# Optimization experiments

Hardware: AMD Instinct MI355X
Metric: run time of the kernel (lower is better)

## Reference

```python
import jax, jax.numpy as jnp
import numpy as np

B, M, N, E, H, HID = 4, 512, 512, 256, 16, 16
D = E // H


def setup_inputs() -> dict:
    key = jax.random.key(0)
    ks = jax.random.split(key, 10)
    u = lambda k, shape, lim: jax.random.uniform(k, shape, jnp.float32, -lim, lim)
    mix1_init = (1.0 / 2.0) ** 0.5
    mix2_init = (1.0 / 16.0) ** 0.5
    return {
        "q_input": jax.random.normal(ks[0], (B, M, E), jnp.float32),
        "kv_input": jax.random.normal(ks[1], (B, N, E), jnp.float32),
        "dmat": jax.random.uniform(ks[2], (B, M, N), jnp.float32),
        "Wq": u(ks[3], (E, E), 1.0 / np.sqrt(E)),
        "Wkv": u(ks[4], (2 * E, E), 1.0 / np.sqrt(E)),
        "mix_W1": u(ks[5], (H, 2, HID), mix1_init),
        "mix_b1": u(ks[6], (H, HID), mix1_init),
        "mix_W2": u(ks[7], (H, HID, 1), mix2_init),
        "mix_b2": u(ks[8], (H, 1), mix2_init),
        "Wout": u(ks[9], (E, E), 1.0 / np.sqrt(E)),
    }


def reference(q_input, kv_input, dmat, Wq, Wkv, mix_W1, mix_b1, mix_W2, mix_b2, Wout):
    b, m, e = q_input.shape
    n = kv_input.shape[1]
    h = mix_W1.shape[0]
    d = e // h
    # projections (torch Linear: y = x @ W.T)
    q = (q_input @ Wq.T).reshape(b, m, h, d).transpose(0, 2, 1, 3)        # b h m d
    kv = (kv_input @ Wkv.T).reshape(b, n, 2, h, d)                        # (two h d) split
    k = kv[:, :, 0].transpose(0, 2, 1, 3)                                 # b h n d
    v = kv[:, :, 1].transpose(0, 2, 1, 3)                                 # b h n d
    scale = jnp.sqrt(jnp.asarray(d, q.dtype))
    scores = jnp.einsum('bhmd,bhnd->bhmn', q, k) / scale                  # b h m n
    # mix scores with dmat via per-head 2-layer MLP on the last (size-2) axis
    mix = jnp.stack([scores, jnp.broadcast_to(dmat[:, None], scores.shape)], axis=-1)  # b h m n 2
    hidden = jax.nn.relu(jnp.einsum('bhmnt,htk->bhmnk', mix, mix_W1)
                         + mix_b1[None, :, None, None, :])                # b h m n HID
    mixed = (jnp.einsum('bhmnk,hko->bhmno', hidden, mix_W2)
             + mix_b2[None, :, None, None, :])[..., 0]                    # b h m n
    probs = jax.nn.softmax(mixed, axis=-1)
    out = jnp.einsum('bhmn,bhnd->bhmd', probs, v)                         # b h m d
    out = out.transpose(0, 2, 1, 3).reshape(b, m, e)                      # b m (h d)
    return out @ Wout.T
```

## Files before the change

### kernel.cpp

```cpp
#include <hip/hip_runtime.h>
#include <stdint.h>
#include <stddef.h>

#define MM 512
#define NN 512
#define EE 256
#define HH 16
#define DD 16

typedef __bf16 bf16x8 __attribute__((ext_vector_type(8)));
typedef float f32x4 __attribute__((ext_vector_type(4)));

static __device__ __forceinline__ bf16x8 bzero8() {
  bf16x8 z;
#pragma unroll
  for (int i = 0; i < 8; ++i) z[i] = (__bf16)0.0f;
  return z;
}

static __device__ __forceinline__ bf16x8 cvt8(const float* __restrict__ p) {
  const float4 u = *(const float4*)p;
  const float4 v = *(const float4*)(p + 4);
  bf16x8 r;
  r[0] = (__bf16)u.x; r[1] = (__bf16)u.y; r[2] = (__bf16)u.z; r[3] = (__bf16)u.w;
  r[4] = (__bf16)v.x; r[5] = (__bf16)v.y; r[6] = (__bf16)v.z; r[7] = (__bf16)v.w;
  return r;
}

static __device__ __forceinline__ unsigned short f2b(float f) {
  union { __bf16 h; unsigned short u; } cv;
  cv.h = (__bf16)f;
  return cv.u;
}

static __device__ __forceinline__ float b2f(unsigned short u) {
  union { unsigned int i; float f; } cv;
  cv.i = ((unsigned int)u) << 16;
  return cv.f;
}

static __device__ __forceinline__ float fexp2(float x) {
  float r;
  asm("v_exp_f32 %0, %1" : "=v"(r) : "v"(x));
  return r;
}

static __device__ __forceinline__ float sload(const float* p) {
  return __int_as_float(__builtin_amdgcn_readfirstlane(__float_as_int(*p)));
}

__global__ __launch_bounds__(256) void proj_all_kernel(
    const float* __restrict__ Xq, const float* __restrict__ Xkv,
    const float* __restrict__ Wq, const float* __restrict__ Wkv,
    const float* __restrict__ Wout,
    unsigned short* __restrict__ Qs, unsigned short* __restrict__ Ks,
    unsigned short* __restrict__ Vt,
    unsigned short* __restrict__ Whi, unsigned short* __restrict__ Wlo) {
  const int by = blockIdx.y;
  const int tid = threadIdx.x;

  if (by == 12) {
    const int base = (blockIdx.x * 256 + tid) * 4;
    const float4 v = *(const float4*)(Wout + base);
    float c[4] = {v.x, v.y, v.z, v.w};
#pragma unroll
    for (int i = 0; i < 4; ++i) {
      const unsigned short hb = f2b(c[i]);
      Whi[base + i] = hb;
      Wlo[base + i] = f2b(c[i] - b2f(hb));
    }
    return;
  }

  const int w = tid >> 6, l = tid & 63;
  const int lg = l >> 4, lr = l & 15;
  const int t0 = blockIdx.x * 32 + (w & 1) * 16;

  if (by < 4) {
    const int n0 = by * 64 + (w >> 1) * 32;
    f32x4 acc0 = {0.f, 0.f, 0.f, 0.f}, acc1 = {0.f, 0.f, 0.f, 0.f};
#pragma unroll
    for (int kc = 0; kc < EE; kc += 32) {
      const int k = kc + lg * 8;
      bf16x8 a  = cvt8(Xq + (size_t)(t0 + lr) * EE + k);
      bf16x8 b0 = cvt8(Wq + (size_t)(n0 + lr) * EE + k);
      bf16x8 b1 = cvt8(Wq + (size_t)(n0 + 16 + lr) * EE + k);
      acc0 = __builtin_amdgcn_mfma_f32_16x16x32_bf16(a, b0, acc0, 0, 0, 0);
      acc1 = __builtin_amdgcn_mfma_f32_16x16x32_bf16(a, b1, acc1, 0, 0, 0);
    }
#pragma unroll
    for (int r = 0; r < 4; ++r) {
      const int t = t0 + 4 * lg + r, b = t >> 9, m = t & 511;
      const int j0 = n0 + lr, j1 = j0 + 16;
      Qs[((size_t)(b * HH + (j0 >> 4)) * MM + m) * DD + (j0 & 15)] = f2b(acc0[r] * 0.25f);
      Qs[((size_t)(b * HH + (j1 >> 4)) * MM + m) * DD + (j1 & 15)] = f2b(acc1[r] * 0.25f);
    }
  } else {
    const int n0 = (by - 4) * 64 + (w >> 1) * 32;
    f32x4 acc0 = {0.f, 0.f, 0.f, 0.f}, acc1 = {0.f, 0.f, 0.f, 0.f};
#pragma unroll
    for (int kc = 0; kc < EE; kc += 32) {
      const int k = kc + lg * 8;
      bf16x8 a  = cvt8(Xkv + (size_t)(t0 + lr) * EE + k);
      bf16x8 b0 = cvt8(Wkv + (size_t)(n0 + lr) * EE + k);
      bf16x8 b1 = cvt8(Wkv + (size_t)(n0 + 16 + lr) * EE + k);
      acc0 = __builtin_amdgcn_mfma_f32_16x16x32_bf16(a, b0, acc0, 0, 0, 0);
      acc1 = __builtin_amdgcn_mfma_f32_16x16x32_bf16(a, b1, acc1, 0, 0, 0);
    }
#pragma unroll
    for (int r = 0; r < 4; ++r) {
      const int t = t0 + 4 * lg + r, b = t >> 9, n = t & 511;
#pragma unroll
      for (int fi = 0; fi < 2; ++fi) {
        const int j = n0 + lr + fi * 16;
        const float v = fi ? acc1[r] : acc0[r];
        if (j < 256) {
          Ks[((size_t)(b * HH + (j >> 4)) * NN + n) * DD + (j & 15)] = f2b(v);
        } else {
          const int jj = j - 256;
          Vt[((size_t)(b * HH + (jj >> 4)) * DD + (jj & 15)) * NN + n] = f2b(v);
        }
      }
    }
  }
}

__global__ __launch_bounds__(256) void attn_kernel(
    const unsigned short* __restrict__ Qs, const unsigned short* __restrict__ Ks,
    const unsigned short* __restrict__ Vt, const float* __restrict__ dmat,
    const float* __restrict__ W1, const float* __restrict__ b1v,
    const float* __restrict__ W2,
    unsigned short* __restrict__ Ahi, unsigned short* __restrict__ Alo) {
  __shared__ unsigned short P[32][520];
  __shared__ float red[4][32];
  __shared__ float pvred[4][2][16][16];

  const int tid = threadIdx.x, w = tid >> 6, l = tid & 63;
  const int lg = l >> 4, lr = l & 15;
  const int bid = blockIdx.x;
  const int mt = bid & 15, hh = (bid >> 4) & 15, b = bid >> 8;
  const int m0 = mt * 32;
  const int n0 = w * 128;

  const unsigned short* Qbase = Qs + ((size_t)(b * HH + hh) * MM + m0) * DD;
  const unsigned short* Kbase = Ks + (size_t)(b * HH + hh) * NN * DD;
  const unsigned short* Vbase = Vt + (size_t)(b * HH + hh) * DD * NN;
  const float* dbase = dmat + (size_t)b * MM * NN;

  bf16x8 qa[2];
#pragma unroll
  for (int mb = 0; mb < 2; ++mb) {
    qa[mb] = bzero8();
    if (lg < 2) qa[mb] = *(const bf16x8*)(Qbase + (mb * 16 + lr) * DD + lg * 8);
  }

  f32x4 zf = {0.f, 0.f, 0.f, 0.f};
  f32x4 c[2][8];
#pragma unroll
  for (int mb = 0; mb < 2; ++mb)
#pragma unroll
    for (int nb = 0; nb < 8; ++nb) c[mb][nb] = zf;

#pragma unroll
  for (int nb = 0; nb < 8; ++nb) {
    bf16x8 kb = bzero8();
    if (lg < 2)
      kb = *(const bf16x8*)(Kbase + (size_t)(n0 + nb * 16 + lr) * DD + lg * 8);
    c[0][nb] = __builtin_amdgcn_mfma_f32_16x16x32_bf16(qa[0], kb, c[0][nb], 0, 0, 0);
    c[1][nb] = __builtin_amdgcn_mfma_f32_16x16x32_bf16(qa[1], kb, c[1][nb], 0, 0, 0);
  }

  float ak[16], ck[16], bk[16], wk[16];
  float Ac = 0.f, Cc = 0.f;
  const float hiln2 = 0.5f * 1.4426950408889634f;
#pragma unroll
  for (int k = 0; k < 16; ++k) {
    ak[k] = sload(W1 + hh * 32 + k);
    ck[k] = sload(W1 + hh * 32 + 16 + k);
    bk[k] = sload(b1v + hh * 16 + k);
    wk[k] = hiln2 * sload(W2 + hh * 16 + k);
    Ac += wk[k] * ak[k];
    Cc += wk[k] * ck[k];
  }

  float psum[2][4] = {};
#pragma unroll
  for (int mb = 0; mb < 2; ++mb) {
    const int mrow = m0 + mb * 16 + 4 * lg;
#pragma unroll
    for (int nb = 0; nb < 8; ++nb) {
      const int ncol = n0 + nb * 16 + lr;
      const float* dp = dbase + (size_t)mrow * NN + ncol;
      float dv[4];
#pragma unroll
      for (int r = 0; r < 4; ++r) dv[r] = dp[(size_t)r * NN];
#pragma unroll
      for (int r = 0; r < 4; ++r) {
        const float s = c[mb][nb][r];
        const float d = dv[r];
        float acc = fmaf(Ac, s, Cc * d);
#pragma unroll
        for (int k = 0; k < 16; ++k) {
          const float t = fmaf(ak[k], s, fmaf(ck[k], d, bk[k]));
          acc = fmaf(wk[k], fabsf(t), acc);
        }
        const float e = fexp2(acc);
        psum[mb][r] += e;
        P[mb * 16 + 4 * lg + r][n0 + nb * 16 + lr] = f2b(e);
      }
    }
  }

#pragma unroll
  for (int mb = 0; mb < 2; ++mb)
#pragma unroll
    for (int r = 0; r < 4; ++r) {
#pragma unroll
      for (int off = 8; off > 0; off >>= 1)
        psum[mb][r] += __shfl_xor(psum[mb][r], off, 16);
      if (lr == 0) red[w][mb * 16 + 4 * lg + r] = psum[mb][r];
    }

  f32x4 pv[2];
  pv[0] = zf; pv[1] = zf;
#pragma unroll
  for (int kb = 0; kb < 4; ++kb) {
    const bf16x8 vb = *(const bf16x8*)(Vbase + (size_t)lr * NN + (n0 + kb * 32 + lg * 8));
#pragma unroll
    for (int mb = 0; mb < 2; ++mb) {
      const bf16x8 pa = *(const bf16x8*)(&P[mb * 16 + lr][n0 + kb * 32 + lg * 8]);
      pv[mb] = __builtin_amdgcn_mfma_f32_16x16x32_bf16(pa, vb, pv[mb], 0, 0, 0);
    }
  }
#pragma unroll
  for (int mb = 0; mb < 2; ++mb)
#pragma unroll
    for (int r = 0; r < 4; ++r) pvred[w][mb][4 * lg + r][lr] = pv[mb][r];
  __syncthreads();

  for (int i = tid; i < 512; i += 256) {
    const int mr = i >> 4, dd = i & 15;
    const float s = pvred[0][mr >> 4][mr & 15][dd] + pvred[1][mr >> 4][mr & 15][dd] +
                    pvred[2][mr >> 4][mr & 15][dd] + pvred[3][mr >> 4][mr & 15][dd];
    const float rs = red[0][mr] + red[1][mr] + red[2][mr] + red[3][mr];
    const float val = s / rs;
    const unsigned short hb = f2b(val);
    const size_t o = ((size_t)(b * MM) + m0 + mr) * EE + hh * DD + dd;
    Ahi[o] = hb;
    Alo[o] = f2b(val - b2f(hb));
  }
}

__global__ __launch_bounds__(256) void out_gemm_kernel(
    const unsigned short* __restrict__ Ahi, const unsigned short* __restrict__ Alo,
    const unsigned short* __restrict__ Whi, const unsigned short* __restrict__ Wlo,
    float* __restrict__ out) {
  const int tid = threadIdx.x, w = tid >> 6, l = tid & 63;
  const int lg = l >> 4, lr = l & 15;
  const int t0 = blockIdx.x * 32 + (w & 1) * 16;
  const int n0 = blockIdx.y * 64 + (w >> 1) * 32;
  f32x4 acc0 = {0.f, 0.f, 0.f, 0.f}, acc1 = {0.f, 0.f, 0.f, 0.f};
#pragma unroll
  for (int kc = 0; kc < EE; kc += 32) {
    const int k = kc + lg * 8;
    const bf16x8 ah = *(const bf16x8*)(Ahi + (size_t)(t0 + lr) * EE + k);
    const bf16x8 al = *(const bf16x8*)(Alo + (size_t)(t0 + lr) * EE + k);
    const bf16x8 bh0 = *(const bf16x8*)(Whi + (size_t)(n0 + lr) * EE + k);
    const bf16x8 bh1 = *(const bf16x8*)(Whi + (size_t)(n0 + 16 + lr) * EE + k);
    const bf16x8 bl0 = *(const bf16x8*)(Wlo + (size_t)(n0 + lr) * EE + k);
    const bf16x8 bl1 = *(const bf16x8*)(Wlo + (size_t)(n0 + 16 + lr) * EE + k);
    acc0 = __builtin_amdgcn_mfma_f32_16x16x32_bf16(ah, bh0, acc0, 0, 0, 0);
    acc0 = __builtin_amdgcn_mfma_f32_16x16x32_bf16(al, bh0, acc0, 0, 0, 0);
    acc0 = __builtin_amdgcn_mfma_f32_16x16x32_bf16(ah, bl0, acc0, 0, 0, 0);
    acc1 = __builtin_amdgcn_mfma_f32_16x16x32_bf16(ah, bh1, acc1, 0, 0, 0);
    acc1 = __builtin_amdgcn_mfma_f32_16x16x32_bf16(al, bh1, acc1, 0, 0, 0);
    acc1 = __builtin_amdgcn_mfma_f32_16x16x32_bf16(ah, bl1, acc1, 0, 0, 0);
  }
#pragma unroll
  for (int r = 0; r < 4; ++r) {
    const int row = t0 + 4 * lg + r;
    out[(size_t)row * EE + n0 + lr] = acc0[r];
    out[(size_t)row * EE + n0 + 16 + lr] = acc1[r];
  }
}

extern "C" void kernel_launch(void* const* d_in, const int* in_sizes, int n_in,
                              void* d_out, int out_size, void* d_ws, size_t ws_size,
                              hipStream_t stream) {
  const float* q_input  = (const float*)d_in[0];
  const float* kv_input = (const float*)d_in[1];
  const float* dmat     = (const float*)d_in[2];
  const float* Wq       = (const float*)d_in[3];
  const float* Wkv      = (const float*)d_in[4];
  const float* W1       = (const float*)d_in[5];
  const float* b1       = (const float*)d_in[6];
  const float* W2       = (const float*)d_in[7];
  const float* Wout     = (const float*)d_in[9];
  float* out = (float*)d_out;

  char* ws = (char*)d_ws;
  unsigned short* Qs  = (unsigned short*)(ws);
  unsigned short* Ks  = (unsigned short*)(ws + (1u << 20));
  unsigned short* Vt  = (unsigned short*)(ws + (2u << 20));
  unsigned short* Ahi = (unsigned short*)(ws + (3u << 20));
  unsigned short* Alo = (unsigned short*)(ws + (4u << 20));
  unsigned short* Whi = (unsigned short*)(ws + (5u << 20));
  unsigned short* Wlo = (unsigned short*)(ws + (5u << 20) + (1u << 17));

  proj_all_kernel<<<dim3(64, 13), 256, 0, stream>>>(q_input, kv_input, Wq, Wkv, Wout,
                                                    Qs, Ks, Vt, Whi, Wlo);
  attn_kernel<<<dim3(1024), 256, 0, stream>>>(Qs, Ks, Vt, dmat, W1, b1, W2, Ahi, Alo);
  out_gemm_kernel<<<dim3(64, 4), 256, 0, stream>>>(Ahi, Alo, Whi, Wlo, out);
}
```

Measured before the change: 63.78 us.

## Refactor mix MLP algebra, transpose score MFMA, fuse per-block S/P loop

```diff
diff --git a/kernel.cpp b/kernel.cpp
--- a/kernel.cpp
+++ b/kernel.cpp
@@ -42,6 +42,12 @@
 static __device__ __forceinline__ float fexp2(float x) {
   float r;
   asm("v_exp_f32 %0, %1" : "=v"(r) : "v"(x));
+  return r;
+}
+
+static __device__ __forceinline__ unsigned int cvtpk(float lo, float hi) {
+  unsigned int r;
+  asm("v_cvt_pk_bf16_f32 %0, %1, %2" : "=v"(r) : "v"(lo), "v"(hi));
   return r;
 }
 
@@ -62,12 +68,12 @@
   if (by == 12) {
     const int base = (blockIdx.x * 256 + tid) * 4;
     const float4 v = *(const float4*)(Wout + base);
-    float c[4] = {v.x, v.y, v.z, v.w};
+    float c4[4] = {v.x, v.y, v.z, v.w};
 #pragma unroll
     for (int i = 0; i < 4; ++i) {
-      const unsigned short hb = f2b(c[i]);
+      const unsigned short hb = f2b(c4[i]);
       Whi[base + i] = hb;
-      Wlo[base + i] = f2b(c[i] - b2f(hb));
+      Wlo[base + i] = f2b(c4[i] - b2f(hb));
     }
     return;
   }
@@ -125,7 +131,7 @@
   }
 }
 
-__global__ __launch_bounds__(256) void attn_kernel(
+__global__ __launch_bounds__(256, 4) void attn_kernel(
     const unsigned short* __restrict__ Qs, const unsigned short* __restrict__ Ks,
     const unsigned short* __restrict__ Vt, const float* __restrict__ dmat,
     const float* __restrict__ W1, const float* __restrict__ b1v,
@@ -133,7 +139,7 @@
     unsigned short* __restrict__ Ahi, unsigned short* __restrict__ Alo) {
   __shared__ unsigned short P[32][520];
   __shared__ float red[4][32];
-  __shared__ float pvred[4][2][16][16];
+  float (*pvred)[2][16][16] = (float (*)[2][16][16]) & P[0][0];
 
   const int tid = threadIdx.x, w = tid >> 6, l = tid & 63;
   const int lg = l >> 4, lr = l & 15;
@@ -147,79 +153,72 @@
   const unsigned short* Vbase = Vt + (size_t)(b * HH + hh) * DD * NN;
   const float* dbase = dmat + (size_t)b * MM * NN;
 
-  bf16x8 qa[2];
-#pragma unroll
-  for (int mb = 0; mb < 2; ++mb) {
-    qa[mb] = bzero8();
-    if (lg < 2) qa[mb] = *(const bf16x8*)(Qbase + (mb * 16 + lr) * DD + lg * 8);
-  }
-
-  f32x4 zf = {0.f, 0.f, 0.f, 0.f};
-  f32x4 c[2][8];
-#pragma unroll
-  for (int mb = 0; mb < 2; ++mb)
-#pragma unroll
-    for (int nb = 0; nb < 8; ++nb) c[mb][nb] = zf;
-
-#pragma unroll
-  for (int nb = 0; nb < 8; ++nb) {
-    bf16x8 kb = bzero8();
-    if (lg < 2)
-      kb = *(const bf16x8*)(Kbase + (size_t)(n0 + nb * 16 + lr) * DD + lg * 8);
-    c[0][nb] = __builtin_amdgcn_mfma_f32_16x16x32_bf16(qa[0], kb, c[0][nb], 0, 0, 0);
-    c[1][nb] = __builtin_amdgcn_mfma_f32_16x16x32_bf16(qa[1], kb, c[1][nb], 0, 0, 0);
-  }
-
-  float ak[16], ck[16], bk[16], wk[16];
+  float ckp[16], bkp[16], wkp[16];
   float Ac = 0.f, Cc = 0.f;
   const float hiln2 = 0.5f * 1.4426950408889634f;
 #pragma unroll
   for (int k = 0; k < 16; ++k) {
-    ak[k] = sload(W1 + hh * 32 + k);
-    ck[k] = sload(W1 + hh * 32 + 16 + k);
-    bk[k] = sload(b1v + hh * 16 + k);
-    wk[k] = hiln2 * sload(W2 + hh * 16 + k);
-    Ac += wk[k] * ak[k];
-    Cc += wk[k] * ck[k];
-  }
-
-  float psum[2][4] = {};
+    const float ak = sload(W1 + hh * 32 + k);
+    const float ck = sload(W1 + hh * 32 + 16 + k);
+    const float bk = sload(b1v + hh * 16 + k);
+    const float wk = hiln2 * sload(W2 + hh * 16 + k);
+    Ac += wk * ak;
+    Cc += wk * ck;
+    const float ra = 1.0f / ak;
+    ckp[k] = ck * ra;
+    bkp[k] = bk * ra;
+    wkp[k] = wk * fabsf(ak);
+  }
+
+  bf16x8 qb[2];
 #pragma unroll
   for (int mb = 0; mb < 2; ++mb) {
-    const int mrow = m0 + mb * 16 + 4 * lg;
-#pragma unroll
-    for (int nb = 0; nb < 8; ++nb) {
-      const int ncol = n0 + nb * 16 + lr;
-      const float* dp = dbase + (size_t)mrow * NN + ncol;
-      float dv[4];
-#pragma unroll
-      for (int r = 0; r < 4; ++r) dv[r] = dp[(size_t)r * NN];
+    qb[mb] = bzero8();
+    if (lg < 2) qb[mb] = *(const bf16x8*)(Qbase + (mb * 16 + lr) * DD + lg * 8);
+  }
+
+  const f32x4 zf = {0.f, 0.f, 0.f, 0.f};
+  float psum[2] = {0.f, 0.f};
+
+#pragma unroll
+  for (int nb = 0; nb < 8; ++nb) {
+    bf16x8 ka = bzero8();
+    if (lg < 2)
+      ka = *(const bf16x8*)(Kbase + (size_t)(n0 + nb * 16 + lr) * DD + lg * 8);
+    f32x4 cc[2];
+    cc[0] = __builtin_amdgcn_mfma_f32_16x16x32_bf16(ka, qb[0], zf, 0, 0, 0);
+    cc[1] = __builtin_amdgcn_mfma_f32_16x16x32_bf16(ka, qb[1], zf, 0, 0, 0);
+#pragma unroll
+    for (int mb = 0; mb < 2; ++mb) {
+      const int mrow = m0 + mb * 16 + lr;
+      const int ncol = n0 + nb * 16 + 4 * lg;
+      const float4 dv = *(const float4*)(dbase + (size_t)mrow * NN + ncol);
+      float ev[4];
 #pragma unroll
       for (int r = 0; r < 4; ++r) {
-        const float s = c[mb][nb][r];
-        const float d = dv[r];
+        const float s = cc[mb][r];
+        const float d = (r == 0) ? dv.x : (r == 1) ? dv.y : (r == 2) ? dv.z : dv.w;
         float acc = fmaf(Ac, s, Cc * d);
 #pragma unroll
-        for (int k = 0; k < 16; ++k) {
-          const float t = fmaf(ak[k], s, fmaf(ck[k], d, bk[k]));
-          acc = fmaf(wk[k], fabsf(t), acc);
-        }
+        for (int k = 0; k < 16; ++k)
+          acc = fmaf(wkp[k], fabsf(s + fmaf(ckp[k], d, bkp[k])), acc);
         const float e = fexp2(acc);
-        psum[mb][r] += e;
-        P[mb * 16 + 4 * lg + r][n0 + nb * 16 + lr] = f2b(e);
+        psum[mb] += e;
+        ev[r] = e;
       }
-    }
-  }
-
-#pragma unroll
-  for (int mb = 0; mb < 2; ++mb)
-#pragma unroll
-    for (int r = 0; r < 4; ++r) {
-#pragma unroll
-      for (int off = 8; off > 0; off >>= 1)
-        psum[mb][r] += __shfl_xor(psum[mb][r], off, 16);
-      if (lr == 0) red[w][mb * 16 + 4 * lg + r] = psum[mb][r];
-    }
+      uint2 u;
+      u.x = cvtpk(ev[0], ev[1]);
+      u.y = cvtpk(ev[2], ev[3]);
+      *(uint2*)&P[mb * 16 + lr][n0 + nb * 16 + 4 * lg] = u;
+    }
+  }
+
+#pragma unroll
+  for (int mb = 0; mb < 2; ++mb) {
+    psum[mb] += __shfl_xor(psum[mb], 16);
+    psum[mb] += __shfl_xor(psum[mb], 32);
+    if (lg == 0) red[w][mb * 16 + lr] = psum[mb];
+  }
 
   f32x4 pv[2];
   pv[0] = zf; pv[1] = zf;
@@ -232,6 +231,7 @@
       pv[mb] = __builtin_amdgcn_mfma_f32_16x16x32_bf16(pa, vb, pv[mb], 0, 0, 0);
     }
   }
+  __syncthreads();
 #pragma unroll
   for (int mb = 0; mb < 2; ++mb)
 #pragma unroll
@@ -257,31 +257,23 @@
     float* __restrict__ out) {
   const int tid = threadIdx.x, w = tid >> 6, l = tid & 63;
   const int lg = l >> 4, lr = l & 15;
-  const int t0 = blockIdx.x * 32 + (w & 1) * 16;
-  const int n0 = blockIdx.y * 64 + (w >> 1) * 32;
-  f32x4 acc0 = {0.f, 0.f, 0.f, 0.f}, acc1 = {0.f, 0.f, 0.f, 0.f};
+  const int t0 = blockIdx.x * 16;
+  const int n0 = blockIdx.y * 64 + w * 16;
+  f32x4 acc = {0.f, 0.f, 0.f, 0.f};
 #pragma unroll
   for (int kc = 0; kc < EE; kc += 32) {
     const int k = kc + lg * 8;
     const bf16x8 ah = *(const bf16x8*)(Ahi + (size_t)(t0 + lr) * EE + k);
     const bf16x8 al = *(const bf16x8*)(Alo + (size_t)(t0 + lr) * EE + k);
-    const bf16x8 bh0 = *(const bf16x8*)(Whi + (size_t)(n0 + lr) * EE + k);
-    const bf16x8 bh1 = *(const bf16x8*)(Whi + (size_t)(n0 + 16 + lr) * EE + k);
-    const bf16x8 bl0 = *(const bf16x8*)(Wlo + (size_t)(n0 + lr) * EE + k);
-    const bf16x8 bl1 = *(const bf16x8*)(Wlo + (size_t)(n0 + 16 + lr) * EE + k);
-    acc0 = __builtin_amdgcn_mfma_f32_16x16x32_bf16(ah, bh0, acc0, 0, 0, 0);
-    acc0 = __builtin_amdgcn_mfma_f32_16x16x32_bf16(al, bh0, acc0, 0, 0, 0);
-    acc0 = __builtin_amdgcn_mfma_f32_16x16x32_bf16(ah, bl0, acc0, 0, 0, 0);
-    acc1 = __builtin_amdgcn_mfma_f32_16x16x32_bf16(ah, bh1, acc1, 0, 0, 0);
-    acc1 = __builtin_amdgcn_mfma_f32_16x16x32_bf16(al, bh1, acc1, 0, 0, 0);
-    acc1 = __builtin_amdgcn_mfma_f32_16x16x32_bf16(ah, bl1, acc1, 0, 0, 0);
-  }
-#pragma unroll
-  for (int r = 0; r < 4; ++r) {
-    const int row = t0 + 4 * lg + r;
-    out[(size_t)row * EE + n0 + lr] = acc0[r];
-    out[(size_t)row * EE + n0 + 16 + lr] = acc1[r];
-  }
+    const bf16x8 bh = *(const bf16x8*)(Whi + (size_t)(n0 + lr) * EE + k);
+    const bf16x8 bl = *(const bf16x8*)(Wlo + (size_t)(n0 + lr) * EE + k);
+    acc = __builtin_amdgcn_mfma_f32_16x16x32_bf16(ah, bh, acc, 0, 0, 0);
+    acc = __builtin_amdgcn_mfma_f32_16x16x32_bf16(al, bh, acc, 0, 0, 0);
+    acc = __builtin_amdgcn_mfma_f32_16x16x32_bf16(ah, bl, acc, 0, 0, 0);
+  }
+#pragma unroll
+  for (int r = 0; r < 4; ++r)
+    out[(size_t)(t0 + 4 * lg + r) * EE + n0 + lr] = acc[r];
 }
 
 extern "C" void kernel_launch(void* const* d_in, const int* in_sizes, int n_in,
@@ -310,5 +302,5 @@
   proj_all_kernel<<<dim3(64, 13), 256, 0, stream>>>(q_input, kv_input, Wq, Wkv, Wout,
                                                     Qs, Ks, Vt, Whi, Wlo);
   attn_kernel<<<dim3(1024), 256, 0, stream>>>(Qs, Ks, Vt, dmat, W1, b1, W2, Ahi, Alo);
-  out_gemm_kernel<<<dim3(64, 4), 256, 0, stream>>>(Ahi, Alo, Whi, Wlo, out);
-}
+  out_gemm_kernel<<<dim3(128, 4), 256, 0, stream>>>(Ahi, Alo, Whi, Wlo, out);
+}
```

Measured after the change: 65.13 us. +2.1%, slower.
